# Optimization experiments

Hardware: AMD Instinct MI355X
Metric: run time of the kernel (lower is better)

The kernel has to match this reference:

```python
import jax, jax.numpy as jnp
import numpy as np

S, T, N, D, H, DT = 4, 4, 65536, 128, 128, 128


def setup_inputs() -> dict:
    key = jax.random.key(0)
    ks = jax.random.split(key, 9)
    inv_d = 1.0 / np.sqrt(D)
    inv_h = 1.0 / np.sqrt(H)
    return {
        "states": jax.random.normal(ks[0], (N, D), dtype=jnp.float32),
        "scores": jax.random.uniform(ks[1], (N, 1), dtype=jnp.float32),
        "type_ids": jax.random.randint(ks[2], (N,), 0, S, dtype=jnp.int32),
        "type_matching": jax.random.normal(ks[3], (S, T), dtype=jnp.float32),
        "W1": jax.random.normal(ks[4], (S, T, D, H), dtype=jnp.float32) * inv_d,
        "b1": jnp.zeros((S, T, H), dtype=jnp.float32),
        "W2": jax.random.normal(ks[5], (S, T, H, DT), dtype=jnp.float32) * inv_h,
        "b2": jnp.zeros((S, T, DT), dtype=jnp.float32),
        "C1": jax.random.normal(ks[6], (S, T, D, H), dtype=jnp.float32) * inv_d,
        "c1": jnp.zeros((S, T, H), dtype=jnp.float32),
        "C2": jax.random.normal(ks[7], (S, T, H, 1), dtype=jnp.float32) * inv_h,
        "c2": jnp.zeros((S, T, 1), dtype=jnp.float32),
    }


def reference(states, scores, type_ids, type_matching, W1, b1, W2, b2, C1, c1, C2, c2):
    """Batched MetaphorMorphism.forward with best_match_only=True.

    For each item with source type s: route to t* = argmax sigmoid(type_matching[s]),
    apply mapper MLP (D->H->DT, ReLU), classifier MLP (D->H->1, ReLU, sigmoid),
    new_score = min(score, classifier_out), item_prob = sigmoid(type_matching)[s, t*].
    """
    match_sig = jax.nn.sigmoid(type_matching)          # [S, T]
    best_t = jnp.argmax(type_matching, axis=1)         # [S] (argmax of sigmoid == argmax of logits)
    best_prob = match_sig[jnp.arange(S), best_t]       # [S]

    out_state = jnp.zeros((states.shape[0], W2.shape[-1]), dtype=states.dtype)
    out_score = jnp.zeros_like(scores)
    # loop over the small, fixed set of source types (structurally distinct experts)
    for s in range(S):
        t = best_t[s]
        h = jax.nn.relu(states @ W1[s, t] + b1[s, t])          # [N, H]
        y = h @ W2[s, t] + b2[s, t]                            # [N, DT]
        hc = jax.nn.relu(states @ C1[s, t] + c1[s, t])         # [N, H]
        cls = jax.nn.sigmoid(hc @ C2[s, t] + c2[s, t])         # [N, 1]
        new_score = jnp.minimum(scores, cls)                   # [N, 1]
        m = (type_ids == s)[:, None]
        out_state = jnp.where(m, y, out_state)
        out_score = jnp.where(m, new_score, out_score)
    item_prob = best_prob[type_ids]                            # [N]
    return out_state, out_score, item_prob
```

## Files before the change

kernel.cpp:

```cpp
#include <hip/hip_runtime.h>
#include <math.h>

#define Nn 65536

typedef short s16x8 __attribute__((ext_vector_type(8)));
typedef float f32x4 __attribute__((ext_vector_type(4)));
typedef unsigned int u32;

__device__ __forceinline__ unsigned short f2bf(float x) {
    u32 u = __float_as_uint(x);
    u += 0x7FFFu + ((u >> 16) & 1u);
    return (unsigned short)(u >> 16);
}

__device__ __forceinline__ int best_t_for(const float* __restrict__ tm, int s, float* mOut) {
    float m = tm[s * 4];
    int am = 0;
#pragma unroll
    for (int j = 1; j < 4; ++j) {
        float v = tm[s * 4 + j];
        if (v > m) { m = v; am = j; }
    }
    if (mOut) *mOut = m;
    return am;
}

__global__ void k_prep(const int* __restrict__ type_ids, const float* __restrict__ tm,
                       const float* __restrict__ W1, const float* __restrict__ W2,
                       const float* __restrict__ C1,
                       int* __restrict__ counts, int* __restrict__ buckets,
                       unsigned short* __restrict__ wbf, float* __restrict__ out_prob) {
    const int tid = threadIdx.x;
    if (blockIdx.x < 64) {
        __shared__ int hist[4];
        __shared__ int off[4];
        __shared__ float prob[4];
        if (tid < 4) {
            hist[tid] = 0;
            float m;
            best_t_for(tm, tid, &m);
            prob[tid] = 1.f / (1.f + expf(-m));
        }
        __syncthreads();
        const int gid = blockIdx.x * 256 + tid;
        int4 ids = ((const int4*)type_ids)[gid];
        float4 p;
        p.x = prob[ids.x]; p.y = prob[ids.y]; p.z = prob[ids.z]; p.w = prob[ids.w];
        ((float4*)out_prob)[gid] = p;
        const int lane = tid & 63;
        int idarr[4] = {ids.x, ids.y, ids.z, ids.w};
#pragma unroll
        for (int j = 0; j < 4; ++j) {
#pragma unroll
            for (int sv = 0; sv < 4; ++sv) {
                unsigned long long m = __ballot(idarr[j] == sv);
                if (lane == 0 && m) atomicAdd(&hist[sv], __popcll(m));
            }
        }
        __syncthreads();
        if (tid < 4) {
            u32 old = atomicCAS((u32*)&counts[tid], 0xAAAAAAAAu, (u32)hist[tid]);
            off[tid] = (old == 0xAAAAAAAAu) ? 0 : atomicAdd(&counts[tid], hist[tid]);
        }
        __syncthreads();
        const int base = gid * 4;
#pragma unroll
        for (int j = 0; j < 4; ++j) {
            int sv = idarr[j];
            int pos = atomicAdd(&off[sv], 1);
            buckets[sv * Nn + pos] = base + j;
        }
    } else {
        int u = (blockIdx.x - 64) * 256 + tid;
        int mat = u >> 11;
        int rr = u & 2047;
        int f = rr >> 6, lane = rr & 63;
        int kk = f >> 3, n8 = f & 7;
        int q = lane >> 4, l15 = lane & 15;
        int sm = mat / 3, w = mat - sm * 3;
        int t = best_t_for(tm, sm, nullptr);
        const float* src = (w == 0) ? W1 : (w == 1) ? W2 : C1;
        const float* sp = src + (((sm * 4 + t) << 14) + n8 * 16 + l15);
        int k0 = kk * 32 + q * 8;
        s16x8 o;
#pragma unroll
        for (int j = 0; j < 8; ++j) o[j] = (short)f2bf(sp[(k0 + j) * 128]);
        *(s16x8*)(wbf + (size_t)u * 8) = o;
    }
}

__global__ __launch_bounds__(256, 2) void k_main(
    const float* __restrict__ states, const float* __restrict__ scores,
    const float* __restrict__ b1g, const float* __restrict__ b2g, const float* __restrict__ c1g,
    const float* __restrict__ tm, const float* __restrict__ C2, const float* __restrict__ c2,
    const int* __restrict__ counts, const int* __restrict__ buckets,
    const unsigned short* __restrict__ wbf,
    float* __restrict__ out_state, float* __restrict__ out_score)
{
    __shared__ __align__(16) unsigned short Abuf[2][64 * 128];
    __shared__ __align__(16) unsigned short Hbuf[64 * 128];
    __shared__ int gIdxLds[2][64];
    __shared__ float scoreLds[2][64];
    __shared__ float pLds[4][64];
    __shared__ float C2s[128];

    const int s = blockIdx.y;
    const int cnt = counts[s];
    const int ntiles = (cnt + 63) >> 6;
    const int bx = blockIdx.x;
    if (bx >= ntiles) return;
    const int t = threadIdx.x;
    const int tt = best_t_for(tm, s, nullptr);
    const int stIdx = s * 4 + tt;

    const int lane = t & 63;
    const int wv = t >> 6;
    const int l15 = lane & 15;
    const int quad = lane >> 4;
    const int myRow = t >> 2;
    const int q4 = t & 3;

    s16x8 wf[3][4][2];
    {
        const unsigned short* wb = wbf + (size_t)s * 3 * 16384;
#pragma unroll
        for (int m = 0; m < 3; ++m)
#pragma unroll
            for (int kk = 0; kk < 4; ++kk)
#pragma unroll
                for (int nn = 0; nn < 2; ++nn)
                    wf[m][kk][nn] = *(const s16x8*)(wb + m * 16384 +
                        (size_t)((kk * 8 + (wv * 2 + nn)) * 64 + lane) * 8);
    }
    if (t >= 128) C2s[t - 128] = C2[stIdx * 128 + (t - 128)];

    float b1v[2], b2v[2], c1v[2];
#pragma unroll
    for (int nn = 0; nn < 2; ++nn) {
        int col = (wv * 2 + nn) * 16 + l15;
        b1v[nn] = b1g[stIdx * 128 + col];
        b2v[nn] = b2g[stIdx * 128 + col];
        c1v[nn] = c1g[stIdx * 128 + col];
    }
    const float c2s = c2[stIdx];

    const int* bkt = buckets + s * Nn;

    {
        int gr = bx * 64 + myRow;
        int g = (gr < cnt) ? bkt[gr] : -1;
        if (q4 == 0) {
            gIdxLds[0][myRow] = g;
            scoreLds[0][myRow] = (g >= 0) ? scores[g] : 0.f;
        }
        unsigned short* dstRow = &Abuf[0][myRow * 128];
        const int rot = (myRow & 15) << 3;
        if (g >= 0) {
            const float4* sp = (const float4*)(states + (size_t)g * 128 + q4 * 32);
            float4 v[8];
#pragma unroll
            for (int i = 0; i < 8; ++i) v[i] = sp[i];
#pragma unroll
            for (int i = 0; i < 8; ++i) {
                int col = (q4 * 32 + i * 4 + rot) & 127;
                ushort4 o;
                o.x = f2bf(v[i].x); o.y = f2bf(v[i].y);
                o.z = f2bf(v[i].z); o.w = f2bf(v[i].w);
                *(ushort4*)(dstRow + col) = o;
            }
        } else {
#pragma unroll
            for (int i = 0; i < 8; ++i) {
                int col = (q4 * 32 + i * 4 + rot) & 127;
                *(ushort4*)(dstRow + col) = ushort4{0, 0, 0, 0};
            }
        }
    }
    int rIdxN = -1;
    if (bx + 128 < ntiles) {
        int gr = (bx + 128) * 64 + myRow;
        rIdxN = (gr < cnt) ? bkt[gr] : -1;
    }
    __syncthreads();

    auto gemm = [&](const unsigned short* Ab, int wm, f32x4 acc[4][2]) {
#pragma unroll
        for (int mg = 0; mg < 4; ++mg)
#pragma unroll
            for (int nn = 0; nn < 2; ++nn) acc[mg][nn] = f32x4{0.f, 0.f, 0.f, 0.f};
#pragma unroll
        for (int kk = 0; kk < 4; ++kk) {
            const int colsw = (kk * 32 + quad * 8 + l15 * 8) & 127;
            s16x8 af[4];
#pragma unroll
            for (int mg = 0; mg < 4; ++mg)
                af[mg] = *(const s16x8*)(Ab + (mg * 16 + l15) * 128 + colsw);
#pragma unroll
            for (int mg = 0; mg < 4; ++mg)
#pragma unroll
                for (int nn = 0; nn < 2; ++nn)
                    acc[mg][nn] = __builtin_amdgcn_mfma_f32_16x16x32_bf16(
                        af[mg], wf[wm][kk][nn], acc[mg][nn], 0, 0, 0);
        }
    };

    f32x4 acc[4][2];
    int cur = 0;
    for (int tile = bx; tile < ntiles; tile += 128, cur ^= 1) {
        const int nxt = cur ^ 1;
        const bool hasNext = (tile + 128) < ntiles;

        gemm(Abuf[cur], 0, acc);
#pragma unroll
        for (int mg = 0; mg < 4; ++mg)
#pragma unroll
            for (int nn = 0; nn < 2; ++nn) {
                int col = (wv * 2 + nn) * 16 + l15;
#pragma unroll
                for (int r = 0; r < 4; ++r) {
                    int row = mg * 16 + quad * 4 + r;
                    float v = fmaxf(acc[mg][nn][r] + b1v[nn], 0.f);
                    Hbuf[row * 128 + ((col + ((row & 15) << 3)) & 127)] = f2bf(v);
                }
            }
        if (q4 == 0) gIdxLds[nxt][myRow] = rIdxN;
        __syncthreads();

        float4 pf[8];
        float scN = 0.f;
        if (hasNext && rIdxN >= 0) {
            const float4* sp = (const float4*)(states + (size_t)rIdxN * 128 + q4 * 32);
#pragma unroll
            for (int i = 0; i < 8; ++i) pf[i] = sp[i];
            scN = scores[rIdxN];
        }
        int rIdxN2 = -1;
        if (tile + 256 < ntiles) {
            int gr = (tile + 256) * 64 + myRow;
            rIdxN2 = (gr < cnt) ? bkt[gr] : -1;
        }

        gemm(Hbuf, 1, acc);
#pragma unroll
        for (int mg = 0; mg < 4; ++mg) {
            int gr4[4];
#pragma unroll
            for (int r = 0; r < 4; ++r) gr4[r] = gIdxLds[cur][mg * 16 + quad * 4 + r];
#pragma unroll
            for (int nn = 0; nn < 2; ++nn) {
                int col = (wv * 2 + nn) * 16 + l15;
                float bias = b2v[nn];
#pragma unroll
                for (int r = 0; r < 4; ++r)
                    if (gr4[r] >= 0) out_state[(size_t)gr4[r] * 128 + col] = acc[mg][nn][r] + bias;
            }
        }

        gemm(Abuf[cur], 2, acc);
        {
            float part[4][4];
#pragma unroll
            for (int mg = 0; mg < 4; ++mg)
#pragma unroll
                for (int r = 0; r < 4; ++r) part[mg][r] = 0.f;
#pragma unroll
            for (int nn = 0; nn < 2; ++nn) {
                int col = (wv * 2 + nn) * 16 + l15;
                float cw = C2s[col];
#pragma unroll
                for (int mg = 0; mg < 4; ++mg)
#pragma unroll
                    for (int r = 0; r < 4; ++r)
                        part[mg][r] += fmaxf(acc[mg][nn][r] + c1v[nn], 0.f) * cw;
            }
#pragma unroll
            for (int off = 1; off < 16; off <<= 1)
#pragma unroll
                for (int mg = 0; mg < 4; ++mg)
#pragma unroll
                    for (int r = 0; r < 4; ++r)
                        part[mg][r] += __shfl_xor(part[mg][r], off, 64);
            if (l15 == 0) {
#pragma unroll
                for (int mg = 0; mg < 4; ++mg)
#pragma unroll
                    for (int r = 0; r < 4; ++r)
                        pLds[wv][mg * 16 + quad * 4 + r] = part[mg][r];
            }
        }

        if (hasNext) {
            unsigned short* dstRow = &Abuf[nxt][myRow * 128];
            const int rot = (myRow & 15) << 3;
            if (rIdxN >= 0) {
#pragma unroll
                for (int i = 0; i < 8; ++i) {
                    int col = (q4 * 32 + i * 4 + rot) & 127;
                    ushort4 o;
                    o.x = f2bf(pf[i].x); o.y = f2bf(pf[i].y);
                    o.z = f2bf(pf[i].z); o.w = f2bf(pf[i].w);
                    *(ushort4*)(dstRow + col) = o;
                }
            } else {
#pragma unroll
                for (int i = 0; i < 8; ++i) {
                    int col = (q4 * 32 + i * 4 + rot) & 127;
                    *(ushort4*)(dstRow + col) = ushort4{0, 0, 0, 0};
                }
            }
            if (q4 == 0) scoreLds[nxt][myRow] = (rIdxN >= 0) ? scN : 0.f;
        }

        int eg = -1;
        float esc = 0.f;
        if (t < 64) { eg = gIdxLds[cur][t]; esc = scoreLds[cur][t]; }
        rIdxN = rIdxN2;
        __syncthreads();

        if (t < 64 && eg >= 0) {
            float tot = pLds[0][t] + pLds[1][t] + pLds[2][t] + pLds[3][t] + c2s;
            float cls = 1.f / (1.f + expf(-tot));
            out_score[eg] = fminf(esc, cls);
        }
    }
}

extern "C" void kernel_launch(void* const* d_in, const int* in_sizes, int n_in,
                              void* d_out, int out_size, void* d_ws, size_t ws_size,
                              hipStream_t stream) {
    const float* states = (const float*)d_in[0];
    const float* scores = (const float*)d_in[1];
    const int*   type_ids = (const int*)d_in[2];
    const float* tm = (const float*)d_in[3];
    const float* W1 = (const float*)d_in[4];
    const float* b1 = (const float*)d_in[5];
    const float* W2 = (const float*)d_in[6];
    const float* b2 = (const float*)d_in[7];
    const float* C1 = (const float*)d_in[8];
    const float* c1 = (const float*)d_in[9];
    const float* C2 = (const float*)d_in[10];
    const float* c2 = (const float*)d_in[11];

    char* ws = (char*)d_ws;
    int*   counts  = (int*)(ws + 0);
    int*   buckets = (int*)(ws + 4096);
    unsigned short* wbf = (unsigned short*)(ws + 1052672);

    float* out_state = (float*)d_out;
    float* out_score = out_state + (size_t)Nn * 128;
    float* out_prob  = out_score + Nn;

    k_prep<<<160, 256, 0, stream>>>(type_ids, tm, W1, W2, C1, counts, buckets, wbf, out_prob);
    k_main<<<dim3(128, 4), 256, 0, stream>>>(states, scores, b1, b2, c1,
        tm, C2, c2, counts, buckets, wbf, out_state, out_score);
}
```

Baseline: 121.1 us.

## Trade register-resident weights and double buffering for higher occupancy and more blocks

The main kernel no longer holds all three weight matrices in registers or double-buffers the activation tile in LDS. Instead it reloads each weight matrix's fragments per tile from the bf16 workspace, single-buffers the gathered states, and runs 3 blocks per CU over a larger grid. The prep kernel now handles one id per thread, bucketing with wave-level ballot prefix sums instead of per-element LDS atomics, and splits the weight conversion across twice as many threads. The aim is more parallelism and latency hiding through occupancy. The cost is repeated weight fragment loads from L2 and the loss of explicit prefetch overlap.

```diff
diff --git a/kernel.cpp b/kernel.cpp
--- a/kernel.cpp
+++ b/kernel.cpp
@@ -31,49 +31,50 @@
                        int* __restrict__ counts, int* __restrict__ buckets,
                        unsigned short* __restrict__ wbf, float* __restrict__ out_prob) {
     const int tid = threadIdx.x;
-    if (blockIdx.x < 64) {
-        __shared__ int hist[4];
-        __shared__ int off[4];
+    if (blockIdx.x < 256) {
         __shared__ float prob[4];
+        __shared__ int waveCnt[4][4];
+        __shared__ int waveBase[4][4];
         if (tid < 4) {
-            hist[tid] = 0;
             float m;
             best_t_for(tm, tid, &m);
             prob[tid] = 1.f / (1.f + expf(-m));
         }
         __syncthreads();
         const int gid = blockIdx.x * 256 + tid;
-        int4 ids = ((const int4*)type_ids)[gid];
-        float4 p;
-        p.x = prob[ids.x]; p.y = prob[ids.y]; p.z = prob[ids.z]; p.w = prob[ids.w];
-        ((float4*)out_prob)[gid] = p;
+        const int id = type_ids[gid];
+        out_prob[gid] = prob[id];
         const int lane = tid & 63;
-        int idarr[4] = {ids.x, ids.y, ids.z, ids.w};
-#pragma unroll
-        for (int j = 0; j < 4; ++j) {
-#pragma unroll
-            for (int sv = 0; sv < 4; ++sv) {
-                unsigned long long m = __ballot(idarr[j] == sv);
-                if (lane == 0 && m) atomicAdd(&hist[sv], __popcll(m));
-            }
+        const int wv = tid >> 6;
+        const unsigned long long lt = (1ull << lane) - 1ull;
+        int myPrefix = 0;
+#pragma unroll
+        for (int sv = 0; sv < 4; ++sv) {
+            unsigned long long m = __ballot(id == sv);
+            if (id == sv) myPrefix = (int)__popcll(m & lt);
+            if (lane == 0) waveCnt[wv][sv] = (int)__popcll(m);
         }
         __syncthreads();
         if (tid < 4) {
-            u32 old = atomicCAS((u32*)&counts[tid], 0xAAAAAAAAu, (u32)hist[tid]);
-            off[tid] = (old == 0xAAAAAAAAu) ? 0 : atomicAdd(&counts[tid], hist[tid]);
-        }
-        __syncthreads();
-        const int base = gid * 4;
-#pragma unroll
-        for (int j = 0; j < 4; ++j) {
-            int sv = idarr[j];
-            int pos = atomicAdd(&off[sv], 1);
-            buckets[sv * Nn + pos] = base + j;
-        }
+            const int sv = tid;
+            int c0 = waveCnt[0][sv], c1 = waveCnt[1][sv];
+            int c2_ = waveCnt[2][sv], c3 = waveCnt[3][sv];
+            int tot = c0 + c1 + c2_ + c3;
+            u32 old = atomicCAS((u32*)&counts[sv], 0xAAAAAAAAu, (u32)tot);
+            int base = (old == 0xAAAAAAAAu) ? 0 : atomicAdd(&counts[sv], tot);
+            waveBase[0][sv] = base;
+            waveBase[1][sv] = base + c0;
+            waveBase[2][sv] = base + c0 + c1;
+            waveBase[3][sv] = base + c0 + c1 + c2_;
+        }
+        __syncthreads();
+        buckets[id * Nn + waveBase[wv][id] + myPrefix] = gid;
     } else {
-        int u = (blockIdx.x - 64) * 256 + tid;
-        int mat = u >> 11;
-        int rr = u & 2047;
+        int v = (blockIdx.x - 256) * 256 + tid;
+        int f_lin = v >> 1;
+        int half = v & 1;
+        int mat = f_lin >> 11;
+        int rr = f_lin & 2047;
         int f = rr >> 6, lane = rr & 63;
         int kk = f >> 3, n8 = f & 7;
         int q = lane >> 4, l15 = lane & 15;
@@ -81,15 +82,17 @@
         int t = best_t_for(tm, sm, nullptr);
         const float* src = (w == 0) ? W1 : (w == 1) ? W2 : C1;
         const float* sp = src + (((sm * 4 + t) << 14) + n8 * 16 + l15);
-        int k0 = kk * 32 + q * 8;
-        s16x8 o;
-#pragma unroll
-        for (int j = 0; j < 8; ++j) o[j] = (short)f2bf(sp[(k0 + j) * 128]);
-        *(s16x8*)(wbf + (size_t)u * 8) = o;
+        int k0 = kk * 32 + q * 8 + half * 4;
+        ushort4 o;
+        o.x = f2bf(sp[(k0 + 0) * 128]);
+        o.y = f2bf(sp[(k0 + 1) * 128]);
+        o.z = f2bf(sp[(k0 + 2) * 128]);
+        o.w = f2bf(sp[(k0 + 3) * 128]);
+        *(ushort4*)(wbf + (size_t)f_lin * 8 + half * 4) = o;
     }
 }
 
-__global__ __launch_bounds__(256, 2) void k_main(
+__global__ __launch_bounds__(256, 3) void k_main(
     const float* __restrict__ states, const float* __restrict__ scores,
     const float* __restrict__ b1g, const float* __restrict__ b2g, const float* __restrict__ c1g,
     const float* __restrict__ tm, const float* __restrict__ C2, const float* __restrict__ c2,
@@ -97,18 +100,17 @@
     const unsigned short* __restrict__ wbf,
     float* __restrict__ out_state, float* __restrict__ out_score)
 {
-    __shared__ __align__(16) unsigned short Abuf[2][64 * 128];
+    __shared__ __align__(16) unsigned short Abuf[64 * 128];
     __shared__ __align__(16) unsigned short Hbuf[64 * 128];
-    __shared__ int gIdxLds[2][64];
-    __shared__ float scoreLds[2][64];
+    __shared__ int gIdxLds[64];
+    __shared__ float scoreLds[64];
     __shared__ float pLds[4][64];
     __shared__ float C2s[128];
 
     const int s = blockIdx.y;
     const int cnt = counts[s];
     const int ntiles = (cnt + 63) >> 6;
-    const int bx = blockIdx.x;
-    if (bx >= ntiles) return;
+    if ((int)blockIdx.x >= ntiles) return;
     const int t = threadIdx.x;
     const int tt = best_t_for(tm, s, nullptr);
     const int stIdx = s * 4 + tt;
@@ -120,18 +122,6 @@
     const int myRow = t >> 2;
     const int q4 = t & 3;
 
-    s16x8 wf[3][4][2];
-    {
-        const unsigned short* wb = wbf + (size_t)s * 3 * 16384;
-#pragma unroll
-        for (int m = 0; m < 3; ++m)
-#pragma unroll
-            for (int kk = 0; kk < 4; ++kk)
-#pragma unroll
-                for (int nn = 0; nn < 2; ++nn)
-                    wf[m][kk][nn] = *(const s16x8*)(wb + m * 16384 +
-                        (size_t)((kk * 8 + (wv * 2 + nn)) * 64 + lane) * 8);
-    }
     if (t >= 128) C2s[t - 128] = C2[stIdx * 128 + (t - 128)];
 
     float b1v[2], b2v[2], c1v[2];
@@ -143,47 +133,19 @@
         c1v[nn] = c1g[stIdx * 128 + col];
     }
     const float c2s = c2[stIdx];
-
     const int* bkt = buckets + s * Nn;
-
-    {
-        int gr = bx * 64 + myRow;
-        int g = (gr < cnt) ? bkt[gr] : -1;
-        if (q4 == 0) {
-            gIdxLds[0][myRow] = g;
-            scoreLds[0][myRow] = (g >= 0) ? scores[g] : 0.f;
-        }
-        unsigned short* dstRow = &Abuf[0][myRow * 128];
-        const int rot = (myRow & 15) << 3;
-        if (g >= 0) {
-            const float4* sp = (const float4*)(states + (size_t)g * 128 + q4 * 32);
-            float4 v[8];
-#pragma unroll
-            for (int i = 0; i < 8; ++i) v[i] = sp[i];
-#pragma unroll
-            for (int i = 0; i < 8; ++i) {
-                int col = (q4 * 32 + i * 4 + rot) & 127;
-                ushort4 o;
-                o.x = f2bf(v[i].x); o.y = f2bf(v[i].y);
-                o.z = f2bf(v[i].z); o.w = f2bf(v[i].w);
-                *(ushort4*)(dstRow + col) = o;
-            }
-        } else {
-#pragma unroll
-            for (int i = 0; i < 8; ++i) {
-                int col = (q4 * 32 + i * 4 + rot) & 127;
-                *(ushort4*)(dstRow + col) = ushort4{0, 0, 0, 0};
-            }
-        }
-    }
-    int rIdxN = -1;
-    if (bx + 128 < ntiles) {
-        int gr = (bx + 128) * 64 + myRow;
-        rIdxN = (gr < cnt) ? bkt[gr] : -1;
-    }
-    __syncthreads();
-
-    auto gemm = [&](const unsigned short* Ab, int wm, f32x4 acc[4][2]) {
+    const unsigned short* wb = wbf + (size_t)s * 3 * 16384;
+
+    auto loadW = [&](int m, s16x8 wf[4][2]) {
+#pragma unroll
+        for (int kk = 0; kk < 4; ++kk)
+#pragma unroll
+            for (int nn = 0; nn < 2; ++nn)
+                wf[kk][nn] = *(const s16x8*)(wb + m * 16384 +
+                    (size_t)((kk * 8 + (wv * 2 + nn)) * 64 + lane) * 8);
+    };
+
+    auto gemm = [&](const unsigned short* Ab, const s16x8 wf[4][2], f32x4 acc[4][2]) {
 #pragma unroll
         for (int mg = 0; mg < 4; ++mg)
 #pragma unroll
@@ -200,17 +162,51 @@
 #pragma unroll
                 for (int nn = 0; nn < 2; ++nn)
                     acc[mg][nn] = __builtin_amdgcn_mfma_f32_16x16x32_bf16(
-                        af[mg], wf[wm][kk][nn], acc[mg][nn], 0, 0, 0);
+                        af[mg], wf[kk][nn], acc[mg][nn], 0, 0, 0);
         }
     };
 
+    s16x8 wfX[4][2], wfY[4][2];
     f32x4 acc[4][2];
-    int cur = 0;
-    for (int tile = bx; tile < ntiles; tile += 128, cur ^= 1) {
-        const int nxt = cur ^ 1;
-        const bool hasNext = (tile + 128) < ntiles;
-
-        gemm(Abuf[cur], 0, acc);
+
+    for (int tile = blockIdx.x; tile < ntiles; tile += gridDim.x) {
+        loadW(0, wfX);
+
+        {
+            int gr = tile * 64 + myRow;
+            int g = (gr < cnt) ? bkt[gr] : -1;
+            if (q4 == 0) {
+                gIdxLds[myRow] = g;
+                scoreLds[myRow] = (g >= 0) ? scores[g] : 0.f;
+            }
+            unsigned short* dstRow = &Abuf[myRow * 128];
+            const int rot = (myRow & 15) << 3;
+            if (g >= 0) {
+                const float4* sp = (const float4*)(states + (size_t)g * 128 + q4 * 32);
+                float4 v[8];
+#pragma unroll
+                for (int i = 0; i < 8; ++i) v[i] = sp[i];
+#pragma unroll
+                for (int i = 0; i < 8; ++i) {
+                    int col = (q4 * 32 + i * 4 + rot) & 127;
+                    ushort4 o;
+                    o.x = f2bf(v[i].x); o.y = f2bf(v[i].y);
+                    o.z = f2bf(v[i].z); o.w = f2bf(v[i].w);
+                    *(ushort4*)(dstRow + col) = o;
+                }
+            } else {
+#pragma unroll
+                for (int i = 0; i < 8; ++i) {
+                    int col = (q4 * 32 + i * 4 + rot) & 127;
+                    *(ushort4*)(dstRow + col) = ushort4{0, 0, 0, 0};
+                }
+            }
+        }
+        __syncthreads();
+
+        loadW(2, wfY);
+
+        gemm(Abuf, wfX, acc);
 #pragma unroll
         for (int mg = 0; mg < 4; ++mg)
 #pragma unroll
@@ -223,29 +219,49 @@
                     Hbuf[row * 128 + ((col + ((row & 15) << 3)) & 127)] = f2bf(v);
                 }
             }
-        if (q4 == 0) gIdxLds[nxt][myRow] = rIdxN;
-        __syncthreads();
-
-        float4 pf[8];
-        float scN = 0.f;
-        if (hasNext && rIdxN >= 0) {
-            const float4* sp = (const float4*)(states + (size_t)rIdxN * 128 + q4 * 32);
-#pragma unroll
-            for (int i = 0; i < 8; ++i) pf[i] = sp[i];
-            scN = scores[rIdxN];
-        }
-        int rIdxN2 = -1;
-        if (tile + 256 < ntiles) {
-            int gr = (tile + 256) * 64 + myRow;
-            rIdxN2 = (gr < cnt) ? bkt[gr] : -1;
-        }
-
-        gemm(Hbuf, 1, acc);
+
+        loadW(1, wfX);
+
+        gemm(Abuf, wfY, acc);
+        {
+            float part[4][4];
+#pragma unroll
+            for (int mg = 0; mg < 4; ++mg)
+#pragma unroll
+                for (int r = 0; r < 4; ++r) part[mg][r] = 0.f;
+#pragma unroll
+            for (int nn = 0; nn < 2; ++nn) {
+                int col = (wv * 2 + nn) * 16 + l15;
+                float cw = C2s[col];
+#pragma unroll
+                for (int mg = 0; mg < 4; ++mg)
+#pragma unroll
+                    for (int r = 0; r < 4; ++r)
+                        part[mg][r] += fmaxf(acc[mg][nn][r] + c1v[nn], 0.f) * cw;
+            }
+#pragma unroll
+            for (int off = 1; off < 16; off <<= 1)
+#pragma unroll
+                for (int mg = 0; mg < 4; ++mg)
+#pragma unroll
+                    for (int r = 0; r < 4; ++r)
+                        part[mg][r] += __shfl_xor(part[mg][r], off, 64);
+            if (l15 == 0) {
+#pragma unroll
+                for (int mg = 0; mg < 4; ++mg)
+#pragma unroll
+                    for (int r = 0; r < 4; ++r)
+                        pLds[wv][mg * 16 + quad * 4 + r] = part[mg][r];
+            }
+        }
+        __syncthreads();
+
+        gemm(Hbuf, wfX, acc);
 #pragma unroll
         for (int mg = 0; mg < 4; ++mg) {
             int gr4[4];
 #pragma unroll
-            for (int r = 0; r < 4; ++r) gr4[r] = gIdxLds[cur][mg * 16 + quad * 4 + r];
+            for (int r = 0; r < 4; ++r) gr4[r] = gIdxLds[mg * 16 + quad * 4 + r];
 #pragma unroll
             for (int nn = 0; nn < 2; ++nn) {
                 int col = (wv * 2 + nn) * 16 + l15;
@@ -256,72 +272,16 @@
             }
         }
 
-        gemm(Abuf[cur], 2, acc);
-        {
-            float part[4][4];
-#pragma unroll
-            for (int mg = 0; mg < 4; ++mg)
-#pragma unroll
-                for (int r = 0; r < 4; ++r) part[mg][r] = 0.f;
-#pragma unroll
-            for (int nn = 0; nn < 2; ++nn) {
-                int col = (wv * 2 + nn) * 16 + l15;
-                float cw = C2s[col];
-#pragma unroll
-                for (int mg = 0; mg < 4; ++mg)
-#pragma unroll
-                    for (int r = 0; r < 4; ++r)
-                        part[mg][r] += fmaxf(acc[mg][nn][r] + c1v[nn], 0.f) * cw;
-            }
-#pragma unroll
-            for (int off = 1; off < 16; off <<= 1)
-#pragma unroll
-                for (int mg = 0; mg < 4; ++mg)
-#pragma unroll
-                    for (int r = 0; r < 4; ++r)
-                        part[mg][r] += __shfl_xor(part[mg][r], off, 64);
-            if (l15 == 0) {
-#pragma unroll
-                for (int mg = 0; mg < 4; ++mg)
-#pragma unroll
-                    for (int r = 0; r < 4; ++r)
-                        pLds[wv][mg * 16 + quad * 4 + r] = part[mg][r];
-            }
-        }
-
-        if (hasNext) {
-            unsigned short* dstRow = &Abuf[nxt][myRow * 128];
-            const int rot = (myRow & 15) << 3;
-            if (rIdxN >= 0) {
-#pragma unroll
-                for (int i = 0; i < 8; ++i) {
-                    int col = (q4 * 32 + i * 4 + rot) & 127;
-                    ushort4 o;
-                    o.x = f2bf(pf[i].x); o.y = f2bf(pf[i].y);
-                    o.z = f2bf(pf[i].z); o.w = f2bf(pf[i].w);
-                    *(ushort4*)(dstRow + col) = o;
-                }
-            } else {
-#pragma unroll
-                for (int i = 0; i < 8; ++i) {
-                    int col = (q4 * 32 + i * 4 + rot) & 127;
-                    *(ushort4*)(dstRow + col) = ushort4{0, 0, 0, 0};
-                }
-            }
-            if (q4 == 0) scoreLds[nxt][myRow] = (rIdxN >= 0) ? scN : 0.f;
-        }
-
-        int eg = -1;
-        float esc = 0.f;
-        if (t < 64) { eg = gIdxLds[cur][t]; esc = scoreLds[cur][t]; }
-        rIdxN = rIdxN2;
-        __syncthreads();
-
-        if (t < 64 && eg >= 0) {
-            float tot = pLds[0][t] + pLds[1][t] + pLds[2][t] + pLds[3][t] + c2s;
-            float cls = 1.f / (1.f + expf(-tot));
-            out_score[eg] = fminf(esc, cls);
-        }
+        if (t < 64) {
+            int eg = gIdxLds[t];
+            if (eg >= 0) {
+                float tot = pLds[0][t] + pLds[1][t] + pLds[2][t] + pLds[3][t] + c2s;
+                float cls = 1.f / (1.f + expf(-tot));
+                out_score[eg] = fminf(scoreLds[t], cls);
+            }
+        }
+
+        if (tile + (int)gridDim.x < ntiles) __syncthreads();
     }
 }
 
@@ -350,7 +310,7 @@
     float* out_score = out_state + (size_t)Nn * 128;
     float* out_prob  = out_score + Nn;
 
-    k_prep<<<160, 256, 0, stream>>>(type_ids, tm, W1, W2, C1, counts, buckets, wbf, out_prob);
-    k_main<<<dim3(128, 4), 256, 0, stream>>>(states, scores, b1, b2, c1,
+    k_prep<<<448, 256, 0, stream>>>(type_ids, tm, W1, W2, C1, counts, buckets, wbf, out_prob);
+    k_main<<<dim3(288, 4), 256, 0, stream>>>(states, scores, b1, b2, c1,
         tm, C2, c2, counts, buckets, wbf, out_state, out_score);
 }
```

Measured after the change: 172.0 us. 1.42x slower.

## Stream per-GEMM weight fragments from global and compute bucket offsets without atomics

Applied to the files above, without the earlier changes.

The main kernel no longer keeps all three weight matrices resident in registers. It reloads one matrix's fragments from global (L2-cached) memory before each GEMM, which frees registers, and the launch bound is raised to 3 blocks per SM for more occupancy. This trades repeated weight reloads on every tile for lower register pressure. The prep kernel now builds bucket positions with wave ballots, prefix popcounts and per-wave count tables instead of per-element LDS atomics, which also makes the bucket order deterministic.

```diff
diff --git a/kernel.cpp b/kernel.cpp
--- a/kernel.cpp
+++ b/kernel.cpp
@@ -32,43 +32,60 @@
                        unsigned short* __restrict__ wbf, float* __restrict__ out_prob) {
     const int tid = threadIdx.x;
     if (blockIdx.x < 64) {
-        __shared__ int hist[4];
-        __shared__ int off[4];
         __shared__ float prob[4];
+        __shared__ int cntL[4][4][4];
+        __shared__ int baseL[4][4];
         if (tid < 4) {
-            hist[tid] = 0;
             float m;
             best_t_for(tm, tid, &m);
             prob[tid] = 1.f / (1.f + expf(-m));
         }
-        __syncthreads();
         const int gid = blockIdx.x * 256 + tid;
         int4 ids = ((const int4*)type_ids)[gid];
+        int idarr[4] = {ids.x, ids.y, ids.z, ids.w};
+        const int lane = tid & 63;
+        const int wv = tid >> 6;
+        const unsigned long long lt = (1ull << lane) - 1ull;
+        unsigned long long msk[4];
+#pragma unroll
+        for (int j = 0; j < 4; ++j) {
+            int idj = idarr[j];
+#pragma unroll
+            for (int sv = 0; sv < 4; ++sv) {
+                unsigned long long m = __ballot(idj == sv);
+                if (idj == sv) msk[j] = m;
+                if (lane == 0) cntL[wv][j][sv] = (int)__popcll(m);
+            }
+        }
+        __syncthreads();
         float4 p;
-        p.x = prob[ids.x]; p.y = prob[ids.y]; p.z = prob[ids.z]; p.w = prob[ids.w];
+        p.x = prob[idarr[0]]; p.y = prob[idarr[1]];
+        p.z = prob[idarr[2]]; p.w = prob[idarr[3]];
         ((float4*)out_prob)[gid] = p;
-        const int lane = tid & 63;
-        int idarr[4] = {ids.x, ids.y, ids.z, ids.w};
-#pragma unroll
-        for (int j = 0; j < 4; ++j) {
-#pragma unroll
-            for (int sv = 0; sv < 4; ++sv) {
-                unsigned long long m = __ballot(idarr[j] == sv);
-                if (lane == 0 && m) atomicAdd(&hist[sv], __popcll(m));
-            }
+        if (tid < 4) {
+            const int sv = tid;
+            int wsum[4];
+#pragma unroll
+            for (int w = 0; w < 4; ++w) {
+                wsum[w] = cntL[w][0][sv] + cntL[w][1][sv] + cntL[w][2][sv] + cntL[w][3][sv];
+            }
+            int tot = wsum[0] + wsum[1] + wsum[2] + wsum[3];
+            u32 old = atomicCAS((u32*)&counts[sv], 0xAAAAAAAAu, (u32)tot);
+            int b = (old == 0xAAAAAAAAu) ? 0 : atomicAdd(&counts[sv], tot);
+#pragma unroll
+            for (int w = 0; w < 4; ++w) { baseL[w][sv] = b; b += wsum[w]; }
         }
         __syncthreads();
-        if (tid < 4) {
-            u32 old = atomicCAS((u32*)&counts[tid], 0xAAAAAAAAu, (u32)hist[tid]);
-            off[tid] = (old == 0xAAAAAAAAu) ? 0 : atomicAdd(&counts[tid], hist[tid]);
-        }
-        __syncthreads();
-        const int base = gid * 4;
+        const int gbase = gid * 4;
 #pragma unroll
         for (int j = 0; j < 4; ++j) {
             int sv = idarr[j];
-            int pos = atomicAdd(&off[sv], 1);
-            buckets[sv * Nn + pos] = base + j;
+            int off = baseL[wv][sv];
+#pragma unroll
+            for (int jp = 0; jp < 4; ++jp)
+                if (jp < j) off += cntL[wv][jp][sv];
+            off += (int)__popcll(msk[j] & lt);
+            buckets[sv * Nn + off] = gbase + j;
         }
     } else {
         int u = (blockIdx.x - 64) * 256 + tid;
@@ -89,7 +106,7 @@
     }
 }
 
-__global__ __launch_bounds__(256, 2) void k_main(
+__global__ __launch_bounds__(256, 3) void k_main(
     const float* __restrict__ states, const float* __restrict__ scores,
     const float* __restrict__ b1g, const float* __restrict__ b2g, const float* __restrict__ c1g,
     const float* __restrict__ tm, const float* __restrict__ C2, const float* __restrict__ c2,
@@ -120,18 +137,6 @@
     const int myRow = t >> 2;
     const int q4 = t & 3;
 
-    s16x8 wf[3][4][2];
-    {
-        const unsigned short* wb = wbf + (size_t)s * 3 * 16384;
-#pragma unroll
-        for (int m = 0; m < 3; ++m)
-#pragma unroll
-            for (int kk = 0; kk < 4; ++kk)
-#pragma unroll
-                for (int nn = 0; nn < 2; ++nn)
-                    wf[m][kk][nn] = *(const s16x8*)(wb + m * 16384 +
-                        (size_t)((kk * 8 + (wv * 2 + nn)) * 64 + lane) * 8);
-    }
     if (t >= 128) C2s[t - 128] = C2[stIdx * 128 + (t - 128)];
 
     float b1v[2], b2v[2], c1v[2];
@@ -143,9 +148,41 @@
         c1v[nn] = c1g[stIdx * 128 + col];
     }
     const float c2s = c2[stIdx];
-
     const int* bkt = buckets + s * Nn;
-
+    const unsigned short* wb = wbf + (size_t)s * 3 * 16384;
+
+    s16x8 wf[4][2];
+    auto loadW = [&](int m) {
+#pragma unroll
+        for (int kk = 0; kk < 4; ++kk)
+#pragma unroll
+            for (int nn = 0; nn < 2; ++nn)
+                wf[kk][nn] = *(const s16x8*)(wb + m * 16384 +
+                    (size_t)((kk * 8 + (wv * 2 + nn)) * 64 + lane) * 8);
+    };
+
+    auto gemm = [&](const unsigned short* Ab, f32x4 acc[4][2]) {
+#pragma unroll
+        for (int mg = 0; mg < 4; ++mg)
+#pragma unroll
+            for (int nn = 0; nn < 2; ++nn) acc[mg][nn] = f32x4{0.f, 0.f, 0.f, 0.f};
+#pragma unroll
+        for (int kk = 0; kk < 4; ++kk) {
+            const int colsw = (kk * 32 + quad * 8 + l15 * 8) & 127;
+            s16x8 af[4];
+#pragma unroll
+            for (int mg = 0; mg < 4; ++mg)
+                af[mg] = *(const s16x8*)(Ab + (mg * 16 + l15) * 128 + colsw);
+#pragma unroll
+            for (int mg = 0; mg < 4; ++mg)
+#pragma unroll
+                for (int nn = 0; nn < 2; ++nn)
+                    acc[mg][nn] = __builtin_amdgcn_mfma_f32_16x16x32_bf16(
+                        af[mg], wf[kk][nn], acc[mg][nn], 0, 0, 0);
+        }
+    };
+
+    loadW(0);
     {
         int gr = bx * 64 + myRow;
         int g = (gr < cnt) ? bkt[gr] : -1;
@@ -183,34 +220,14 @@
     }
     __syncthreads();
 
-    auto gemm = [&](const unsigned short* Ab, int wm, f32x4 acc[4][2]) {
-#pragma unroll
-        for (int mg = 0; mg < 4; ++mg)
-#pragma unroll
-            for (int nn = 0; nn < 2; ++nn) acc[mg][nn] = f32x4{0.f, 0.f, 0.f, 0.f};
-#pragma unroll
-        for (int kk = 0; kk < 4; ++kk) {
-            const int colsw = (kk * 32 + quad * 8 + l15 * 8) & 127;
-            s16x8 af[4];
-#pragma unroll
-            for (int mg = 0; mg < 4; ++mg)
-                af[mg] = *(const s16x8*)(Ab + (mg * 16 + l15) * 128 + colsw);
-#pragma unroll
-            for (int mg = 0; mg < 4; ++mg)
-#pragma unroll
-                for (int nn = 0; nn < 2; ++nn)
-                    acc[mg][nn] = __builtin_amdgcn_mfma_f32_16x16x32_bf16(
-                        af[mg], wf[wm][kk][nn], acc[mg][nn], 0, 0, 0);
-        }
-    };
-
     f32x4 acc[4][2];
     int cur = 0;
     for (int tile = bx; tile < ntiles; tile += 128, cur ^= 1) {
         const int nxt = cur ^ 1;
         const bool hasNext = (tile + 128) < ntiles;
 
-        gemm(Abuf[cur], 0, acc);
+        gemm(Abuf[cur], acc);
+        loadW(1);
 #pragma unroll
         for (int mg = 0; mg < 4; ++mg)
 #pragma unroll
@@ -240,7 +257,8 @@
             rIdxN2 = (gr < cnt) ? bkt[gr] : -1;
         }
 
-        gemm(Hbuf, 1, acc);
+        gemm(Hbuf, acc);
+        loadW(2);
 #pragma unroll
         for (int mg = 0; mg < 4; ++mg) {
             int gr4[4];
@@ -256,7 +274,8 @@
             }
         }
 
-        gemm(Abuf[cur], 2, acc);
+        gemm(Abuf[cur], acc);
+        loadW(0);
         {
             float part[4][4];
 #pragma unroll
```

Result: slower. 163.8 us (+35.3%).
